# Optimization experiments

Measured on AMD Instinct MI355X. Metric: run time of the kernel, lower is better.

Reference implementation:

```python
import jax, jax.numpy as jnp
import numpy as np


def _dequant4(qweight, scales, qzeros, groupsize):
    """GPTQ int4 dequant.
    qweight: (K//8, N) int32, 8 int4 values packed along K (low nibble = lowest k).
    scales:  (G, N) float, G = K // groupsize.
    qzeros:  (G, N//8) int32, 8 int4 zeros packed along N.
    Returns dense (K, N) float weight: w*scale - (z+1)*scale, per the kernel.
    """
    K8, N = qweight.shape
    shifts = jnp.arange(8, dtype=jnp.int32) * 4
    # unpack weights along K: (K//8, 8, N) -> (K, N)
    w = (qweight[:, None, :] >> shifts[None, :, None]) & 15
    w = w.reshape(K8 * 8, N).astype(scales.dtype)
    # unpack zeros along N: (G, N//8, 8) -> (G, N)
    z = (qzeros[:, :, None] >> shifts[None, None, :]) & 15
    z = z.reshape(qzeros.shape[0], N).astype(scales.dtype)
    zero_term = (z + 1.0) * scales  # (G, N)
    # broadcast each group's scale/zero over its groupsize rows of K
    sc_k = jnp.repeat(scales, groupsize, axis=0)      # (K, N)
    zt_k = jnp.repeat(zero_term, groupsize, axis=0)   # (K, N)
    return w * sc_k - zt_k


def setup_inputs() -> dict:
    key = jax.random.key(0)
    ks = jax.random.split(key, 10)
    B, S, K, N = 2, 2048, 4096, 11008
    gs = 128
    G_gu = K // gs        # 32
    G_d = N // gs         # 86
    hi = jnp.int32(1073741823)
    x = jax.random.normal(ks[0], (B, S, K), dtype=jnp.float32)
    gate_qweight = jax.random.randint(ks[1], (K // 8, N), 0, hi, dtype=jnp.int32)
    gate_scales = jax.random.uniform(ks[2], (G_gu, N), dtype=jnp.float32) * 0.01
    gate_qzeros = jax.random.randint(ks[3], (G_gu, N // 8), 0, hi, dtype=jnp.int32)
    up_qweight = jax.random.randint(ks[4], (K // 8, N), 0, hi, dtype=jnp.int32)
    up_scales = jax.random.uniform(ks[5], (G_gu, N), dtype=jnp.float32) * 0.01
    up_qzeros = jax.random.randint(ks[6], (G_gu, N // 8), 0, hi, dtype=jnp.int32)
    down_qweight = jax.random.randint(ks[7], (N // 8, K), 0, hi, dtype=jnp.int32)
    down_scales = jax.random.uniform(ks[8], (G_d, K), dtype=jnp.float32) * 0.01
    down_qzeros = jax.random.randint(ks[9], (G_d, K // 8), 0, hi, dtype=jnp.int32)
    return {
        "x": x,
        "gate_qweight": gate_qweight, "gate_scales": gate_scales, "gate_qzeros": gate_qzeros,
        "up_qweight": up_qweight, "up_scales": up_scales, "up_qzeros": up_qzeros,
        "down_qweight": down_qweight, "down_scales": down_scales, "down_qzeros": down_qzeros,
        "groupsize": gs,
    }


def reference(x, gate_qweight, gate_scales, gate_qzeros,
              up_qweight, up_scales, up_qzeros,
              down_qweight, down_scales, down_qzeros, groupsize):
    Wg = _dequant4(gate_qweight, gate_scales, gate_qzeros, groupsize)  # (K, N)
    Wu = _dequant4(up_qweight, up_scales, up_qzeros, groupsize)        # (K, N)
    g = jnp.einsum('bsk,kn->bsn', x, Wg)
    u = jnp.einsum('bsk,kn->bsn', x, Wu)
    h = jax.nn.silu(g) * u                                             # (B, S, N)
    Wd = _dequant4(down_qweight, down_scales, down_qzeros, groupsize)  # (N, K)
    return jnp.einsum('bsn,nk->bsk', h, Wd)
```

## Files before the change

kernel.cpp:

```cpp
#include <hip/hip_runtime.h>
#include <hip/hip_bf16.h>

static constexpr int M  = 4096;
static constexpr int K  = 4096;
static constexpr int NN = 11008;

typedef _Float16 f16;
typedef _Float16 f16x2 __attribute__((ext_vector_type(2)));
typedef _Float16 f16x8 __attribute__((ext_vector_type(8)));
typedef float    f32x4 __attribute__((ext_vector_type(4)));

union dq_u { f16x2 h[4]; f16x8 v; };

__device__ __forceinline__ f16x8 dq8(unsigned q, f16x2 s2, f16x2 zc2) {
    dq_u u;
    unsigned t0 = ( q         & 0x000F000Fu) | 0x64006400u;
    unsigned t1 = ((q >> 4)   & 0x000F000Fu) | 0x64006400u;
    unsigned t2 = ((q >> 8)   & 0x000F000Fu) | 0x64006400u;
    unsigned t3 = ((q >> 12)  & 0x000F000Fu) | 0x64006400u;
    u.h[0] = (__builtin_bit_cast(f16x2, t0) - zc2) * s2;
    u.h[1] = (__builtin_bit_cast(f16x2, t1) - zc2) * s2;
    u.h[2] = (__builtin_bit_cast(f16x2, t2) - zc2) * s2;
    u.h[3] = (__builtin_bit_cast(f16x2, t3) - zc2) * s2;
    return u.v;
}

__device__ __forceinline__ void gll16(const f16* g, f16* l) {
    __builtin_amdgcn_global_load_lds(
        (const __attribute__((address_space(1))) unsigned int*)g,
        (__attribute__((address_space(3))) unsigned int*)l,
        16, 0, 0);
}

__global__ __launch_bounds__(256) void convert_x_kernel(
    const float* __restrict__ x, f16* __restrict__ xp)
{
    size_t i = ((size_t)blockIdx.x * 256 + threadIdx.x) * 8;
    float4 f0 = *(const float4*)(x + i);
    float4 f1 = *(const float4*)(x + i + 4);
    f16x8 v;
    v[0] = (f16)f0.x; v[1] = (f16)f1.x;
    v[2] = (f16)f0.y; v[3] = (f16)f1.y;
    v[4] = (f16)f0.z; v[5] = (f16)f1.z;
    v[6] = (f16)f0.w; v[7] = (f16)f1.w;
    *(f16x8*)(xp + i) = v;
}

__global__ __launch_bounds__(256) void dequant_gu_strip(
    const int* __restrict__ gqw, const float* __restrict__ gsc, const int* __restrict__ gqz,
    const int* __restrict__ uqw, const float* __restrict__ usc, const int* __restrict__ uqz,
    f16* __restrict__ wc, int n0)
{
    int nl = blockIdx.x * 256 + threadIdx.x;
    int n  = n0 + nl;
    int k0 = blockIdx.y * 32;
    int g  = k0 >> 7;
    int sh = (n & 7) * 4;

    float sgf = gsc[(size_t)g * NN + n];
    float suf = usc[(size_t)g * NN + n];
    int zg = (gqz[(size_t)g * (NN / 8) + (n >> 3)] >> sh) & 15;
    int zu = (uqz[(size_t)g * (NN / 8) + (n >> 3)] >> sh) & 15;
    f16 sgh = (f16)sgf, suh = (f16)suf;
    f16 zcg = (f16)(float)(1025 + zg);
    f16 zcu = (f16)(float)(1025 + zu);
    f16x2 s2g = {sgh, sgh}, zc2g = {zcg, zcg};
    f16x2 s2u = {suh, suh}, zc2u = {zcu, zcu};

    size_t jg = (size_t)((nl >> 4) * 32 + (nl & 15));
    size_t ju = jg + 16;

#pragma unroll
    for (int i = 0; i < 4; ++i) {
        unsigned qg = (unsigned)gqw[(size_t)(k0 / 8 + i) * NN + n];
        unsigned qu = (unsigned)uqw[(size_t)(k0 / 8 + i) * NN + n];
        *(f16x8*)&wc[jg * K + k0 + i * 8] = dq8(qg, s2g, zc2g);
        *(f16x8*)&wc[ju * K + k0 + i * 8] = dq8(qu, s2u, zc2u);
    }
}

__global__ __launch_bounds__(256) void dequant_d_strip(
    const int* __restrict__ dqw, const float* __restrict__ dsc, const int* __restrict__ dqz,
    f16* __restrict__ wd, int c0)
{
    int cl = blockIdx.x * 256 + threadIdx.x;
    int c  = c0 + cl;
    int n0 = blockIdx.y * 32;
    int g  = n0 >> 7;
    int sh = (c & 7) * 4;

    float sf = dsc[(size_t)g * K + c];
    int   z  = (dqz[(size_t)g * (K / 8) + (c >> 3)] >> sh) & 15;
    f16 shh = (f16)sf;
    f16 zch = (f16)(float)(1025 + z);
    f16x2 s2 = {shh, shh}, zc2 = {zch, zch};

#pragma unroll
    for (int i = 0; i < 4; ++i) {
        unsigned q = (unsigned)dqw[(size_t)(n0 / 8 + i) * K + c];
        *(f16x8*)&wd[(size_t)cl * NN + n0 + i * 8] = dq8(q, s2, zc2);
    }
}

template<int EPI>
__global__ __launch_bounds__(512) void gemm8p(
    const f16* __restrict__ Ag,
    const f16* __restrict__ Bg,
    void*      __restrict__ Cv,
    const int SK, const int NT, const int cbase)
{
    __shared__ __align__(16) f16 LA[2][2][128 * 64];
    __shared__ __align__(16) f16 LB[2][2][128 * 64];

    const int tid  = threadIdx.x;
    const int lane = tid & 63;
    const int wave = tid >> 6;
    const int wm   = wave >> 2;
    const int wbh  = (wave >> 1) & 1;
    const int wnq  = wave & 1;
    const int quad = lane >> 4;
    const int lr   = lane & 15;

    const int GX  = gridDim.x, GY = gridDim.y;
    const int nwg = GX * GY;
    const int lin = blockIdx.y * GX + blockIdx.x;
    const int q8  = nwg >> 3, r8 = nwg & 7;
    const int xcd = lin & 7, ldx = lin >> 3;
    const int s   = (xcd < r8 ? xcd * (q8 + 1)
                              : r8 * (q8 + 1) + (xcd - r8) * q8) + ldx;
    const int span = 4 * GY;
    const int mb   = (s / span) * 4 + (s & 3);
    const int cb   = (s % span) >> 2;

    const int m0  = mb * 256;
    const int nb0 = cb * 256;

    const int trow = tid >> 3;
    const int tch  = (tid & 7) ^ (trow & 7);
    const size_t arow = (size_t)(m0  + trow) * SK + (size_t)tch * 8;
    const size_t brow = (size_t)(nb0 + trow) * SK + (size_t)tch * 8;
    const int lstg = wave * 512;

    const int c0e = ((quad) ^ (lr & 7)) * 8;
    const int c1e = ((4 + quad) ^ (lr & 7)) * 8;

    f32x4 acc[8][4];
#pragma unroll
    for (int i = 0; i < 8; ++i)
#pragma unroll
        for (int j = 0; j < 4; ++j) acc[i][j] = (f32x4){0.f, 0.f, 0.f, 0.f};

    f16x8 a_[2][4];
    f16x8 b_[2][2][2];

#define STAGE_A(D_, H_, T_) do {                                              \
    const f16* s_ = Ag + arow + (size_t)(H_) * 128 * SK + (size_t)(T_) * 64;  \
    gll16(s_, &LA[D_][H_][lstg]);                                             \
    gll16(s_ + (size_t)64 * SK, &LA[D_][H_][4096 + lstg]); } while (0)

#define STAGE_B(D_, H_, T_) do {                                              \
    const f16* s_ = Bg + brow + (size_t)(H_) * 128 * SK + (size_t)(T_) * 64;  \
    gll16(s_, &LB[D_][H_][lstg]);                                             \
    gll16(s_ + (size_t)64 * SK, &LB[D_][H_][4096 + lstg]); } while (0)

#define LOAD_A(D_, MH_) do {                                                  \
    _Pragma("unroll")                                                         \
    for (int mt = 0; mt < 4; ++mt) {                                          \
        a_[0][mt] = *(const f16x8*)&LA[D_][wm][((MH_) * 64 + mt * 16 + lr) * 64 + c0e]; \
        a_[1][mt] = *(const f16x8*)&LA[D_][wm][((MH_) * 64 + mt * 16 + lr) * 64 + c1e]; \
    } } while (0)

#define LOAD_B(D_, NH_) do {                                                  \
    _Pragma("unroll")                                                         \
    for (int n2 = 0; n2 < 2; ++n2) {                                          \
        b_[NH_][0][n2] = *(const f16x8*)&LB[D_][wbh][(wnq * 64 + (NH_) * 32 + n2 * 16 + lr) * 64 + c0e]; \
        b_[NH_][1][n2] = *(const f16x8*)&LB[D_][wbh][(wnq * 64 + (NH_) * 32 + n2 * 16 + lr) * 64 + c1e]; \
    } } while (0)

#define QMFMA(MH_, NH_) do {                                                  \
    __builtin_amdgcn_s_setprio(1);                                            \
    _Pragma("unroll")                                                         \
    for (int kk = 0; kk < 2; ++kk)                                            \
    _Pragma("unroll")                                                         \
    for (int n2 = 0; n2 < 2; ++n2)                                            \
    _Pragma("unroll")                                                         \
    for (int mt = 0; mt < 4; ++mt)                                            \
        acc[(MH_) * 4 + mt][(NH_) * 2 + n2] =                                 \
            __builtin_amdgcn_mfma_f32_16x16x32_f16(                           \
                a_[kk][mt], b_[NH_][kk][n2],                                  \
                acc[(MH_) * 4 + mt][(NH_) * 2 + n2], 0, 0, 0);                \
    __builtin_amdgcn_s_setprio(0); } while (0)

#define BAR() do { __builtin_amdgcn_s_barrier();                              \
                   __builtin_amdgcn_sched_barrier(0); } while (0)
#define WAITV6() do { asm volatile("s_waitcnt vmcnt(6)" ::: "memory");        \
                      __builtin_amdgcn_sched_barrier(0); } while (0)
#define WAITV0() do { asm volatile("s_waitcnt vmcnt(0)" ::: "memory");        \
                      __builtin_amdgcn_sched_barrier(0); } while (0)

    STAGE_A(0, 0, 0); STAGE_A(0, 1, 0); STAGE_B(0, 0, 0); STAGE_B(0, 1, 0);
    if (NT > 1) { STAGE_B(1, 0, 1); STAGE_A(1, 0, 1); STAGE_A(1, 1, 1); }
    if (NT > 1) { WAITV6(); } else { WAITV0(); }
    BAR();

#pragma unroll 2
    for (int t = 0; t < NT; ++t) {
        const int d  = t & 1;
        const int dn = d ^ 1;
        const bool s1 = (t + 1 < NT);
        const bool s2 = (t + 2 < NT);

        LOAD_A(d, 0);
        LOAD_B(d, 0);
        if (s1) STAGE_B(dn, 1, t + 1);
        QMFMA(0, 0);
        BAR();
        LOAD_B(d, 1);
        QMFMA(0, 1);
        BAR();
        LOAD_A(d, 1);
        if (s2) STAGE_B(d, 0, t + 2);
        QMFMA(1, 0);
        BAR();
        if (s2) { STAGE_A(d, 0, t + 2); STAGE_A(d, 1, t + 2); }
        QMFMA(1, 1);
        if (s2) { WAITV6(); } else { WAITV0(); }
        BAR();
    }

    if constexpr (EPI == 0) {
        f16* __restrict__ h = (f16*)Cv;
        const int jw = cbase + nb0 + wbh * 128 + wnq * 64;
#pragma unroll
        for (int p = 0; p < 2; ++p) {
            const int nbase = ((jw + p * 32) >> 5) * 16;
            const int n  = nbase + lr;
            const int np = (n & ~7) | (((n & 3) << 1) | ((n >> 2) & 1));
#pragma unroll
            for (int mt8 = 0; mt8 < 8; ++mt8)
#pragma unroll
                for (int r = 0; r < 4; ++r) {
                    const int m = m0 + wm * 128 + mt8 * 16 + quad * 4 + r;
                    float gv = acc[mt8][2 * p][r];
                    float uv = acc[mt8][2 * p + 1][r];
                    float hv = (gv / (1.0f + __expf(-gv))) * uv;
                    h[(size_t)m * NN + np] = (f16)hv;
                }
        }
    } else {
        float* __restrict__ out = (float*)Cv;
        const int cw = cbase + nb0 + wbh * 128 + wnq * 64;
#pragma unroll
        for (int nt = 0; nt < 4; ++nt)
#pragma unroll
            for (int mt8 = 0; mt8 < 8; ++mt8)
#pragma unroll
                for (int r = 0; r < 4; ++r) {
                    const int m = m0 + wm * 128 + mt8 * 16 + quad * 4 + r;
                    out[(size_t)m * K + cw + nt * 16 + lr] = acc[mt8][nt][r];
                }
    }

#undef STAGE_A
#undef STAGE_B
#undef LOAD_A
#undef LOAD_B
#undef QMFMA
#undef BAR
#undef WAITV6
#undef WAITV0
}

extern "C" void kernel_launch(void* const* d_in, const int* in_sizes, int n_in,
                              void* d_out, int out_size, void* d_ws, size_t ws_size,
                              hipStream_t stream) {
    const float* x   = (const float*)d_in[0];
    const int*   gqw = (const int*)d_in[1];
    const float* gsc = (const float*)d_in[2];
    const int*   gqz = (const int*)d_in[3];
    const int*   uqw = (const int*)d_in[4];
    const float* usc = (const float*)d_in[5];
    const int*   uqz = (const int*)d_in[6];
    const int*   dqw = (const int*)d_in[7];
    const float* dsc = (const float*)d_in[8];
    const int*   dqz = (const int*)d_in[9];
    float* out = (float*)d_out;

    const size_t HB = (size_t)M * NN * 2;
    char* ws = (char*)d_ws;
    f16* h  = (f16*)ws;
    f16* xp = (f16*)(ws + HB);

    convert_x_kernel<<<(M * K / 8) / 256, 256, 0, stream>>>(x, xp);

    const int JC = 8192;
    for (int j0 = 0; j0 < 2 * NN; j0 += JC) {
        int jc  = 2 * NN - j0 < JC ? 2 * NN - j0 : JC;
        int n0  = j0 >> 1;
        int ncn = jc >> 1;
        f16* wc = (f16*)d_out;
        dequant_gu_strip<<<dim3(ncn / 256, K / 32), 256, 0, stream>>>(
            gqw, gsc, gqz, uqw, usc, uqz, wc, n0);
        gemm8p<0><<<dim3(M / 256, jc / 256), 512, 0, stream>>>(
            xp, wc, (void*)h, K, K / 64, j0);
    }

    size_t availD = ws_size - HB;
    int KC = (int)(availD / ((size_t)NN * 2));
    KC &= ~255;
    if (KC > K) KC = K;
    if (KC < 256) KC = 256;
    f16* wd = (f16*)(ws + HB);
    for (int c0 = 0; c0 < K; c0 += KC) {
        int kc = K - c0 < KC ? K - c0 : KC;
        dequant_d_strip<<<dim3(kc / 256, NN / 32), 256, 0, stream>>>(
            dqw, dsc, dqz, wd, c0);
        gemm8p<1><<<dim3(M / 256, kc / 256), 512, 0, stream>>>(
            h, wd, out, NN, NN / 64, c0);
    }
}
```

Measured before the change: 1.329 ms.

## Fuse int4 dequantization into GEMM B-tile loading, dropping separate dequant passes

The separate dequant kernels that wrote fp16 weight strips to global memory are gone. Each GEMM block now loads packed int4 weights, scales and zeros directly, dequantizes them in registers and writes the fp16 tile into shared memory in the swizzled layout. This removes the global write and re-read of the dense weights and the chunked launch loops, so each GEMM runs as a single launch. In exchange, every M-block repeats the dequant work, register pressure rises, and the B path now uses synchronous loads into registers instead of async global-to-LDS copies, which can stall the pipeline.

```diff
diff --git a/kernel.cpp b/kernel.cpp
--- a/kernel.cpp
+++ b/kernel.cpp
@@ -46,68 +46,13 @@
     *(f16x8*)(xp + i) = v;
 }
 
-__global__ __launch_bounds__(256) void dequant_gu_strip(
-    const int* __restrict__ gqw, const float* __restrict__ gsc, const int* __restrict__ gqz,
-    const int* __restrict__ uqw, const float* __restrict__ usc, const int* __restrict__ uqz,
-    f16* __restrict__ wc, int n0)
-{
-    int nl = blockIdx.x * 256 + threadIdx.x;
-    int n  = n0 + nl;
-    int k0 = blockIdx.y * 32;
-    int g  = k0 >> 7;
-    int sh = (n & 7) * 4;
-
-    float sgf = gsc[(size_t)g * NN + n];
-    float suf = usc[(size_t)g * NN + n];
-    int zg = (gqz[(size_t)g * (NN / 8) + (n >> 3)] >> sh) & 15;
-    int zu = (uqz[(size_t)g * (NN / 8) + (n >> 3)] >> sh) & 15;
-    f16 sgh = (f16)sgf, suh = (f16)suf;
-    f16 zcg = (f16)(float)(1025 + zg);
-    f16 zcu = (f16)(float)(1025 + zu);
-    f16x2 s2g = {sgh, sgh}, zc2g = {zcg, zcg};
-    f16x2 s2u = {suh, suh}, zc2u = {zcu, zcu};
-
-    size_t jg = (size_t)((nl >> 4) * 32 + (nl & 15));
-    size_t ju = jg + 16;
-
-#pragma unroll
-    for (int i = 0; i < 4; ++i) {
-        unsigned qg = (unsigned)gqw[(size_t)(k0 / 8 + i) * NN + n];
-        unsigned qu = (unsigned)uqw[(size_t)(k0 / 8 + i) * NN + n];
-        *(f16x8*)&wc[jg * K + k0 + i * 8] = dq8(qg, s2g, zc2g);
-        *(f16x8*)&wc[ju * K + k0 + i * 8] = dq8(qu, s2u, zc2u);
-    }
-}
-
-__global__ __launch_bounds__(256) void dequant_d_strip(
-    const int* __restrict__ dqw, const float* __restrict__ dsc, const int* __restrict__ dqz,
-    f16* __restrict__ wd, int c0)
-{
-    int cl = blockIdx.x * 256 + threadIdx.x;
-    int c  = c0 + cl;
-    int n0 = blockIdx.y * 32;
-    int g  = n0 >> 7;
-    int sh = (c & 7) * 4;
-
-    float sf = dsc[(size_t)g * K + c];
-    int   z  = (dqz[(size_t)g * (K / 8) + (c >> 3)] >> sh) & 15;
-    f16 shh = (f16)sf;
-    f16 zch = (f16)(float)(1025 + z);
-    f16x2 s2 = {shh, shh}, zc2 = {zch, zch};
-
-#pragma unroll
-    for (int i = 0; i < 4; ++i) {
-        unsigned q = (unsigned)dqw[(size_t)(n0 / 8 + i) * K + c];
-        *(f16x8*)&wd[(size_t)cl * NN + n0 + i * 8] = dq8(q, s2, zc2);
-    }
-}
-
 template<int EPI>
 __global__ __launch_bounds__(512) void gemm8p(
     const f16* __restrict__ Ag,
-    const f16* __restrict__ Bg,
+    const int* __restrict__ qwG, const float* __restrict__ scG, const int* __restrict__ qzG,
+    const int* __restrict__ qwU, const float* __restrict__ scU, const int* __restrict__ qzU,
     void*      __restrict__ Cv,
-    const int SK, const int NT, const int cbase)
+    const int SK, const int NT)
 {
     __shared__ __align__(16) f16 LA[2][2][128 * 64];
     __shared__ __align__(16) f16 LB[2][2][128 * 64];
@@ -137,9 +82,32 @@
 
     const int trow = tid >> 3;
     const int tch  = (tid & 7) ^ (trow & 7);
-    const size_t arow = (size_t)(m0  + trow) * SK + (size_t)tch * 8;
-    const size_t brow = (size_t)(nb0 + trow) * SK + (size_t)tch * 8;
+    const size_t arow = (size_t)(m0 + trow) * SK + (size_t)tch * 8;
     const int lstg = wave * 512;
+
+    const int RS  = (EPI == 0) ? NN : K;
+    const int brL = tid & 127;
+    const int bk8 = tid >> 7;
+    const int*   qwp[2]; const float* scp[2]; const int* qzp[2];
+    size_t qoff[2], soff[2], zoff[2]; int zsh[2];
+#pragma unroll
+    for (int h = 0; h < 2; ++h) {
+        int j = nb0 + h * 128 + brL;
+        int nc;
+        if constexpr (EPI == 0) {
+            nc = ((j >> 5) << 4) | (j & 15);
+            int gu = (j >> 4) & 1;
+            qwp[h] = gu ? qwU : qwG;
+            scp[h] = gu ? scU : scG;
+            qzp[h] = gu ? qzU : qzG;
+        } else {
+            nc = j; qwp[h] = qwG; scp[h] = scG; qzp[h] = qzG;
+        }
+        qoff[h] = (size_t)bk8 * RS + nc;
+        soff[h] = nc;
+        zoff[h] = nc >> 3;
+        zsh[h]  = (nc & 7) * 4;
+    }
 
     const int c0e = ((quad) ^ (lr & 7)) * 8;
     const int c1e = ((4 + quad) ^ (lr & 7)) * 8;
@@ -152,16 +120,38 @@
 
     f16x8 a_[2][4];
     f16x8 b_[2][2][2];
+    unsigned qr[2][2]; float scr[2]; unsigned zr[2]; f16x8 bval[2][2];
 
 #define STAGE_A(D_, H_, T_) do {                                              \
     const f16* s_ = Ag + arow + (size_t)(H_) * 128 * SK + (size_t)(T_) * 64;  \
     gll16(s_, &LA[D_][H_][lstg]);                                             \
     gll16(s_ + (size_t)64 * SK, &LA[D_][H_][4096 + lstg]); } while (0)
 
-#define STAGE_B(D_, H_, T_) do {                                              \
-    const f16* s_ = Bg + brow + (size_t)(H_) * 128 * SK + (size_t)(T_) * 64;  \
-    gll16(s_, &LB[D_][H_][lstg]);                                             \
-    gll16(s_ + (size_t)64 * SK, &LB[D_][H_][4096 + lstg]); } while (0)
+#define ISSUEB(T_) do {                                                       \
+    _Pragma("unroll")                                                         \
+    for (int h = 0; h < 2; ++h) {                                             \
+        qr[h][0] = (unsigned)qwp[h][(size_t)((T_) * 8) * RS + qoff[h]];       \
+        qr[h][1] = (unsigned)qwp[h][(size_t)((T_) * 8 + 4) * RS + qoff[h]];   \
+        scr[h]   = scp[h][(size_t)((T_) >> 1) * RS + soff[h]];                \
+        zr[h]    = (unsigned)qzp[h][(size_t)((T_) >> 1) * (RS >> 3) + zoff[h]]; \
+    } } while (0)
+
+#define DQB() do {                                                            \
+    _Pragma("unroll")                                                         \
+    for (int h = 0; h < 2; ++h) {                                             \
+        f16 sh_ = (f16)scr[h];                                                \
+        f16 zc_ = (f16)(float)(1025 + (int)((zr[h] >> zsh[h]) & 15u));        \
+        f16x2 s2_ = {sh_, sh_}, zc2_ = {zc_, zc_};                            \
+        bval[h][0] = dq8(qr[h][0], s2_, zc2_);                                \
+        bval[h][1] = dq8(qr[h][1], s2_, zc2_);                                \
+    } } while (0)
+
+#define WRITEB(D_) do {                                                       \
+    _Pragma("unroll")                                                         \
+    for (int h = 0; h < 2; ++h) {                                             \
+        *(f16x8*)&LB[D_][h][brL * 64 + ((bk8 ^ (brL & 7)) * 8)]       = bval[h][0]; \
+        *(f16x8*)&LB[D_][h][brL * 64 + (((bk8 + 4) ^ (brL & 7)) * 8)] = bval[h][1]; \
+    } } while (0)
 
 #define LOAD_A(D_, MH_) do {                                                  \
     _Pragma("unroll")                                                         \
@@ -193,44 +183,44 @@
 
 #define BAR() do { __builtin_amdgcn_s_barrier();                              \
                    __builtin_amdgcn_sched_barrier(0); } while (0)
-#define WAITV6() do { asm volatile("s_waitcnt vmcnt(6)" ::: "memory");        \
-                      __builtin_amdgcn_sched_barrier(0); } while (0)
+#define LGKM0() do { asm volatile("s_waitcnt lgkmcnt(0)" ::: "memory");       \
+                     __builtin_amdgcn_sched_barrier(0); } while (0)
 #define WAITV0() do { asm volatile("s_waitcnt vmcnt(0)" ::: "memory");        \
                       __builtin_amdgcn_sched_barrier(0); } while (0)
 
-    STAGE_A(0, 0, 0); STAGE_A(0, 1, 0); STAGE_B(0, 0, 0); STAGE_B(0, 1, 0);
-    if (NT > 1) { STAGE_B(1, 0, 1); STAGE_A(1, 0, 1); STAGE_A(1, 1, 1); }
-    if (NT > 1) { WAITV6(); } else { WAITV0(); }
-    BAR();
+    ISSUEB(0); DQB(); WRITEB(0);
+    ISSUEB(1); DQB(); WRITEB(1);
+    STAGE_A(0, 0, 0); STAGE_A(0, 1, 0);
+    STAGE_A(1, 0, 1); STAGE_A(1, 1, 1);
+    LGKM0(); WAITV0(); BAR();
 
 #pragma unroll 2
     for (int t = 0; t < NT; ++t) {
         const int d  = t & 1;
-        const int dn = d ^ 1;
-        const bool s1 = (t + 1 < NT);
         const bool s2 = (t + 2 < NT);
 
+        if (s2) ISSUEB(t + 2);
         LOAD_A(d, 0);
         LOAD_B(d, 0);
-        if (s1) STAGE_B(dn, 1, t + 1);
         QMFMA(0, 0);
         BAR();
         LOAD_B(d, 1);
         QMFMA(0, 1);
         BAR();
         LOAD_A(d, 1);
-        if (s2) STAGE_B(d, 0, t + 2);
+        if (s2) DQB();
         QMFMA(1, 0);
         BAR();
-        if (s2) { STAGE_A(d, 0, t + 2); STAGE_A(d, 1, t + 2); }
+        if (s2) { WRITEB(d); STAGE_A(d, 0, t + 2); STAGE_A(d, 1, t + 2); }
         QMFMA(1, 1);
-        if (s2) { WAITV6(); } else { WAITV0(); }
+        if (s2) { LGKM0(); }
+        else if (t + 1 < NT) { WAITV0(); }
         BAR();
     }
 
     if constexpr (EPI == 0) {
         f16* __restrict__ h = (f16*)Cv;
-        const int jw = cbase + nb0 + wbh * 128 + wnq * 64;
+        const int jw = nb0 + wbh * 128 + wnq * 64;
 #pragma unroll
         for (int p = 0; p < 2; ++p) {
             const int nbase = ((jw + p * 32) >> 5) * 16;
@@ -249,7 +239,7 @@
         }
     } else {
         float* __restrict__ out = (float*)Cv;
-        const int cw = cbase + nb0 + wbh * 128 + wnq * 64;
+        const int cw = nb0 + wbh * 128 + wnq * 64;
 #pragma unroll
         for (int nt = 0; nt < 4; ++nt)
 #pragma unroll
@@ -262,12 +252,14 @@
     }
 
 #undef STAGE_A
-#undef STAGE_B
+#undef ISSUEB
+#undef DQB
+#undef WRITEB
 #undef LOAD_A
 #undef LOAD_B
 #undef QMFMA
 #undef BAR
-#undef WAITV6
+#undef LGKM0
 #undef WAITV0
 }
 
@@ -293,29 +285,9 @@
 
     convert_x_kernel<<<(M * K / 8) / 256, 256, 0, stream>>>(x, xp);
 
-    const int JC = 8192;
-    for (int j0 = 0; j0 < 2 * NN; j0 += JC) {
-        int jc  = 2 * NN - j0 < JC ? 2 * NN - j0 : JC;
-        int n0  = j0 >> 1;
-        int ncn = jc >> 1;
-        f16* wc = (f16*)d_out;
-        dequant_gu_strip<<<dim3(ncn / 256, K / 32), 256, 0, stream>>>(
-            gqw, gsc, gqz, uqw, usc, uqz, wc, n0);
-        gemm8p<0><<<dim3(M / 256, jc / 256), 512, 0, stream>>>(
-            xp, wc, (void*)h, K, K / 64, j0);
-    }
-
-    size_t availD = ws_size - HB;
-    int KC = (int)(availD / ((size_t)NN * 2));
-    KC &= ~255;
-    if (KC > K) KC = K;
-    if (KC < 256) KC = 256;
-    f16* wd = (f16*)(ws + HB);
-    for (int c0 = 0; c0 < K; c0 += KC) {
-        int kc = K - c0 < KC ? K - c0 : KC;
-        dequant_d_strip<<<dim3(kc / 256, NN / 32), 256, 0, stream>>>(
-            dqw, dsc, dqz, wd, c0);
-        gemm8p<1><<<dim3(M / 256, kc / 256), 512, 0, stream>>>(
-            h, wd, out, NN, NN / 64, c0);
-    }
-}
+    gemm8p<0><<<dim3(M / 256, (2 * NN) / 256), 512, 0, stream>>>(
+        xp, gqw, gsc, gqz, uqw, usc, uqz, (void*)h, K, K / 64);
+
+    gemm8p<1><<<dim3(M / 256, K / 256), 512, 0, stream>>>(
+        h, dqw, dsc, dqz, dqw, dsc, dqz, (void*)out, NN, NN / 64);
+}
```

Measured after the change: 1.566 ms. 1.18x slower.
